# Kernel optimization log

Hardware: AMD Instinct MI355X
Metric: run time of the kernel (lower is better)

Reference implementation:

```python
import jax, jax.numpy as jnp
from jax import lax
import numpy as np

VOCAB, IN_DIM, MEM_DIM, SEQ = 100000, 256, 512, 2048
PAD = 0


def setup_inputs() -> dict:
    key = jax.random.key(0)
    k = jax.random.split(key, 7)
    emb = jax.random.normal(k[0], (VOCAB, IN_DIM), dtype=jnp.float32)
    emb = emb.at[PAD].set(0.0)  # padding_idx row is zero
    s_ih = 1.0 / np.sqrt(IN_DIM)
    s_hh = 1.0 / np.sqrt(MEM_DIM)
    return {
        "linputs": jax.random.randint(k[1], (SEQ,), 0, VOCAB, dtype=jnp.int64),
        "rinputs": jax.random.randint(k[2], (SEQ,), 0, VOCAB, dtype=jnp.int64),
        "emb": emb,
        "W_ih": jax.random.normal(k[3], (4 * MEM_DIM, IN_DIM), dtype=jnp.float32) * s_ih,
        "W_hh": jax.random.normal(k[4], (4 * MEM_DIM, MEM_DIM), dtype=jnp.float32) * s_hh,
        "b_ih": jax.random.normal(k[5], (4 * MEM_DIM,), dtype=jnp.float32) * s_hh,
        "b_hh": jax.random.normal(k[6], (4 * MEM_DIM,), dtype=jnp.float32) * s_hh,
    }


def _lstm_last_h(x_seq, W_ih, W_hh, b):
    # x_seq: [S, in_dim]. Returns h_T [mem_dim]. PyTorch gate order: i, f, g, o.
    H = W_hh.shape[1]
    # precompute input projections for all timesteps (one big GEMM)
    xp = x_seq @ W_ih.T + b  # [S, 4H]
    def step(carry, xg):
        h, c = carry
        gates = xg + h @ W_hh.T  # [4H]
        i = jax.nn.sigmoid(gates[:H])
        f = jax.nn.sigmoid(gates[H:2 * H])
        g = jnp.tanh(gates[2 * H:3 * H])
        o = jax.nn.sigmoid(gates[3 * H:])
        c = f * c + i * g
        h = o * jnp.tanh(c)
        return (h, c), None
    init = (jnp.zeros((H,), x_seq.dtype), jnp.zeros((H,), x_seq.dtype))
    (h, _), _ = lax.scan(step, init, xp)
    return h


def reference(linputs, rinputs, emb, W_ih, W_hh, b_ih, b_hh):
    b = b_ih + b_hh
    lx = emb[linputs]  # [S, in_dim]
    rx = emb[rinputs]
    lh = _lstm_last_h(lx, W_ih, W_hh, b)
    rh = _lstm_last_h(rx, W_ih, W_hh, b)
    return jnp.exp(-jnp.sum(jnp.abs(lh - rh)))
```

## Files before the change

kernel.cpp:

```cpp
#include <hip/hip_runtime.h>
#include <hip/hip_bf16.h>

#define SEQL  2048
#define IND   256
#define MEMD  512
#define G4    2048
#define NWG   16
#define VOCABN 100000

typedef __attribute__((ext_vector_type(4))) unsigned uintx4;
typedef __attribute__((ext_vector_type(2))) _Float16 half2v;

__device__ __forceinline__ unsigned short f2h_bits(float f) {
  _Float16 h = (_Float16)f;
  return __builtin_bit_cast(unsigned short, h);
}
__device__ __forceinline__ float h2f(unsigned bits) {
  return (float)__builtin_bit_cast(_Float16, (unsigned short)(bits & 0xffffu));
}

template <int CTRL>
__device__ __forceinline__ float dpp_fold_add(float v) {
  int x = __builtin_amdgcn_update_dpp(0, __float_as_int(v), CTRL, 0xf, 0xf, true);
  return v + __int_as_float(x);
}

__global__ void init_k(unsigned* __restrict__ hbuf) {
  int i = blockIdx.x * blockDim.x + threadIdx.x;
  if (i < 2 * 2 * MEMD) hbuf[i] = 0u;
}

__global__ __launch_bounds__(256) void xp_gemm(
    const int* __restrict__ lin, const int* __restrict__ rin,
    const float* __restrict__ emb, const float* __restrict__ W_ih,
    const float* __restrict__ b_ih, const float* __restrict__ b_hh,
    unsigned short* __restrict__ xp) {
  __shared__ float As[64][68];
  __shared__ float Bs[64][68];
  const int s = blockIdx.z;
  const int* ids = (s == 0) ? lin : rin;
  const int t0 = blockIdx.x * 64;
  const int n0 = blockIdx.y * 64;
  const int tid = threadIdx.x;
  const int tx = tid & 15, ty = tid >> 4;

  float acc[4][4];
#pragma unroll
  for (int i = 0; i < 4; ++i)
#pragma unroll
    for (int j = 0; j < 4; ++j) acc[i][j] = 0.f;

  for (int kc = 0; kc < IND; kc += 64) {
#pragma unroll
    for (int j = 0; j < 4; ++j) {
      int fi  = tid + 256 * j;
      int row = fi >> 4;
      int c4  = fi & 15;
      int id  = ids[t0 + row];
      id = max(0, min(id, VOCABN - 1));
      const float4 va = *(const float4*)(emb + (size_t)id * IND + kc + c4 * 4);
      As[c4 * 4 + 0][row] = va.x; As[c4 * 4 + 1][row] = va.y;
      As[c4 * 4 + 2][row] = va.z; As[c4 * 4 + 3][row] = va.w;
      const float4 vb = *(const float4*)(W_ih + (size_t)(n0 + row) * IND + kc + c4 * 4);
      Bs[c4 * 4 + 0][row] = vb.x; Bs[c4 * 4 + 1][row] = vb.y;
      Bs[c4 * 4 + 2][row] = vb.z; Bs[c4 * 4 + 3][row] = vb.w;
    }
    __syncthreads();
#pragma unroll 8
    for (int k = 0; k < 64; ++k) {
      const float4 a = *(const float4*)&As[k][tx * 4];
      const float4 b = *(const float4*)&Bs[k][ty * 4];
      acc[0][0] = fmaf(a.x, b.x, acc[0][0]); acc[0][1] = fmaf(a.x, b.y, acc[0][1]);
      acc[0][2] = fmaf(a.x, b.z, acc[0][2]); acc[0][3] = fmaf(a.x, b.w, acc[0][3]);
      acc[1][0] = fmaf(a.y, b.x, acc[1][0]); acc[1][1] = fmaf(a.y, b.y, acc[1][1]);
      acc[1][2] = fmaf(a.y, b.z, acc[1][2]); acc[1][3] = fmaf(a.y, b.w, acc[1][3]);
      acc[2][0] = fmaf(a.z, b.x, acc[2][0]); acc[2][1] = fmaf(a.z, b.y, acc[2][1]);
      acc[2][2] = fmaf(a.z, b.z, acc[2][2]); acc[2][3] = fmaf(a.z, b.w, acc[2][3]);
      acc[3][0] = fmaf(a.w, b.x, acc[3][0]); acc[3][1] = fmaf(a.w, b.y, acc[3][1]);
      acc[3][2] = fmaf(a.w, b.z, acc[3][2]); acc[3][3] = fmaf(a.w, b.w, acc[3][3]);
    }
    __syncthreads();
  }
#pragma unroll
  for (int ri = 0; ri < 4; ++ri) {
#pragma unroll
    for (int bj = 0; bj < 4; ++bj) {
      int t = t0 + tx * 4 + ri;
      int n = n0 + ty * 4 + bj;
      float v = acc[ri][bj] + b_ih[n] + b_hh[n];
      int w = (n & 511) >> 5;
      int gate = n >> 9;
      int hd = n & 31;
      int pos = w * 128 + hd * 4 + gate;
      xp[((size_t)s * SEQL + t) * G4 + pos] = f2h_bits(v);
    }
  }
}

__global__ __launch_bounds__(512, 2) void lstm_rec(
    const float* __restrict__ W_hh,
    const unsigned short* __restrict__ xp,
    unsigned* __restrict__ hbuf) {
  __shared__ unsigned hlds[16 * 20];
  const int blk = blockIdx.x;
  const int s = blk & 1;
  const int w = blk >> 1;
  const int tid = threadIdx.x;
  const int lane = tid & 63;
  const int wv = tid >> 6;
  const int cg = tid & 15;
  const int rg = tid >> 4;

  half2v wreg[4][16];
#pragma unroll
  for (int g = 0; g < 4; ++g) {
    const float* src = W_hh + ((size_t)g * MEMD + w * 32 + rg) * MEMD + cg * 32;
#pragma unroll
    for (int q = 0; q < 8; ++q) {
      const float4 v = *(const float4*)(src + q * 4);
      half2v p0; p0.x = (_Float16)v.x; p0.y = (_Float16)v.y;
      half2v p1; p1.x = (_Float16)v.z; p1.y = (_Float16)v.w;
      wreg[g][q * 2 + 0] = p0;
      wreg[g][q * 2 + 1] = p1;
    }
  }

  unsigned* hbase = hbuf + s * (2 * MEMD);
  const unsigned short* xq0 = xp + (size_t)s * SEQL * G4 + w * 128 + rg * 4;
  float cst = 0.f;

  ushort4 xg_cur = *(const ushort4*)xq0;

  for (int t = 0; t < SEQL; ++t) {
    ushort4 xg_next;
    {
      int tn = (t + 1 < SEQL) ? t + 1 : t;
      xg_next = *(const ushort4*)(xq0 + (size_t)tn * G4);
    }

    if (wv == 0) {
      const unsigned* hr = hbase + (t & 1) * MEMD + 8 * lane;
      unsigned long long a0 = (unsigned long long)hr;
      unsigned long long a1 = (unsigned long long)(hr + 4);
      uintx4 va, vb;
      const unsigned want = (unsigned)t;
      int guard = 0;
      for (;;) {
        asm volatile(
            "global_load_dwordx4 %0, %2, off sc0 sc1\n\t"
            "global_load_dwordx4 %1, %3, off sc0 sc1\n\t"
            "s_waitcnt vmcnt(0)"
            : "=&v"(va), "=&v"(vb)
            : "v"(a0), "v"(a1)
            : "memory");
        bool good = (va.x >> 16) == want && (va.y >> 16) == want &&
                    (va.z >> 16) == want && (va.w >> 16) == want &&
                    (vb.x >> 16) == want && (vb.y >> 16) == want &&
                    (vb.z >> 16) == want && (vb.w >> 16) == want;
        if (__all(good)) break;
        if (++guard > (1 << 16)) break;
      }
      uintx4 pk;
      pk.x = (va.x & 0xffffu) | (va.y << 16);
      pk.y = (va.z & 0xffffu) | (va.w << 16);
      pk.z = (vb.x & 0xffffu) | (vb.y << 16);
      pk.w = (vb.z & 0xffffu) | (vb.w << 16);
      *(uintx4*)&hlds[(lane >> 2) * 20 + (lane & 3) * 4] = pk;
    }
    __syncthreads();

    half2v hp[16];
    {
      const uintx4* hq = (const uintx4*)&hlds[cg * 20];
#pragma unroll
      for (int q = 0; q < 4; ++q) {
        uintx4 u = hq[q];
        hp[q * 4 + 0] = __builtin_bit_cast(half2v, u.x);
        hp[q * 4 + 1] = __builtin_bit_cast(half2v, u.y);
        hp[q * 4 + 2] = __builtin_bit_cast(half2v, u.z);
        hp[q * 4 + 3] = __builtin_bit_cast(half2v, u.w);
      }
    }
    float part[4] = {0.f, 0.f, 0.f, 0.f};
#pragma unroll
    for (int p = 0; p < 16; ++p) {
#pragma unroll
      for (int g = 0; g < 4; ++g)
        part[g] = __builtin_amdgcn_fdot2(wreg[g][p], hp[p], part[g], false);
    }
#pragma unroll
    for (int g = 0; g < 4; ++g) {
      part[g] = dpp_fold_add<0xB1>(part[g]);
      part[g] = dpp_fold_add<0x4E>(part[g]);
      part[g] = dpp_fold_add<0x141>(part[g]);
      part[g] = dpp_fold_add<0x140>(part[g]);
    }

    float gi = part[0] + h2f(xg_cur.x);
    float gf = part[1] + h2f(xg_cur.y);
    float gg = part[2] + h2f(xg_cur.z);
    float go = part[3] + h2f(xg_cur.w);
    float i_ = 1.f / (1.f + __expf(-gi));
    float f_ = 1.f / (1.f + __expf(-gf));
    float ggc = fminf(fmaxf(gg, -15.f), 15.f);
    float e2 = __expf(-2.f * ggc);
    float g_ = (1.f - e2) / (1.f + e2);
    float o_ = 1.f / (1.f + __expf(-go));
    cst = f_ * cst + i_ * g_;
    float cc = fminf(fmaxf(cst, -15.f), 15.f);
    float e2c = __expf(-2.f * cc);
    float th = (1.f - e2c) / (1.f + e2c);
    float h_ = o_ * th;

    unsigned pw = (((unsigned)(t + 1)) << 16) | (unsigned)f2h_bits(h_);
    unsigned q1 = __shfl(pw, 16, 64);
    unsigned q2 = __shfl(pw, 32, 64);
    unsigned q3 = __shfl(pw, 48, 64);
    if (lane == 0) {
      uintx4 val;
      val.x = pw; val.y = q1; val.z = q2; val.w = q3;
      unsigned long long addr =
          (unsigned long long)(hbase + ((t + 1) & 1) * MEMD + w * 32 + wv * 4);
      asm volatile("global_store_dwordx4 %0, %1, off sc0 sc1"
                   :: "v"(addr), "v"(val) : "memory");
    }
    xg_cur = xg_next;
  }
}

__global__ __launch_bounds__(512) void finish_k(const unsigned* __restrict__ hbuf,
                                                float* __restrict__ out) {
  const int tid = threadIdx.x;
  float l = h2f(hbuf[tid]);
  float r = h2f(hbuf[2 * MEMD + tid]);
  float d = fabsf(l - r);
#pragma unroll
  for (int m = 32; m >= 1; m >>= 1) d += __shfl_xor(d, m, 64);
  __shared__ float wsum[8];
  if ((tid & 63) == 0) wsum[tid >> 6] = d;
  __syncthreads();
  if (tid == 0) {
    float sum = 0.f;
#pragma unroll
    for (int i = 0; i < 8; ++i) sum += wsum[i];
    out[0] = expf(-sum);
  }
}

extern "C" void kernel_launch(void* const* d_in, const int* in_sizes, int n_in,
                              void* d_out, int out_size, void* d_ws, size_t ws_size,
                              hipStream_t stream) {
  const int*   lin  = (const int*)d_in[0];
  const int*   rin  = (const int*)d_in[1];
  const float* emb  = (const float*)d_in[2];
  const float* W_ih = (const float*)d_in[3];
  const float* W_hh = (const float*)d_in[4];
  const float* b_ih = (const float*)d_in[5];
  const float* b_hh = (const float*)d_in[6];
  float* out = (float*)d_out;

  unsigned char* ws = (unsigned char*)d_ws;
  unsigned short* xp = (unsigned short*)ws;
  unsigned* hbuf = (unsigned*)(ws + (size_t)2 * SEQL * G4 * sizeof(unsigned short));

  hipLaunchKernelGGL(init_k, dim3(2), dim3(1024), 0, stream, hbuf);
  hipLaunchKernelGGL(xp_gemm, dim3(SEQL / 64, G4 / 64, 2), dim3(256), 0, stream,
                     lin, rin, emb, W_ih, b_ih, b_hh, xp);
  hipLaunchKernelGGL(lstm_rec, dim3(2 * NWG), dim3(512), 0, stream, W_hh, xp, hbuf);
  hipLaunchKernelGGL(finish_k, dim3(1), dim3(512), 0, stream, hbuf, out);
}
```

Measured before the change: 3.661 ms.

## Use 8 workgroups of 1024 threads per sequence for the LSTM recurrence

Each sequence's recurrence now runs on 8 workgroups of 1024 threads instead of 16 of 512. Each workgroup owns 64 hidden units, and the xp gate layout is permuted to match. Halving the number of cooperating workgroups reduces the cross-workgroup polling and synchronisation traffic at every timestep. The hidden-state gather is split across two waves. The cost is larger per-workgroup __syncthreads barriers and higher register pressure at 1024 threads per block.

```diff
diff --git a/kernel.cpp b/kernel.cpp
--- a/kernel.cpp
+++ b/kernel.cpp
@@ -5,7 +5,7 @@
 #define IND   256
 #define MEMD  512
 #define G4    2048
-#define NWG   16
+#define NWGS  8
 #define VOCABN 100000
 
 typedef __attribute__((ext_vector_type(4))) unsigned uintx4;
@@ -88,16 +88,16 @@
       int t = t0 + tx * 4 + ri;
       int n = n0 + ty * 4 + bj;
       float v = acc[ri][bj] + b_ih[n] + b_hh[n];
-      int w = (n & 511) >> 5;
+      int w = (n & 511) >> 6;
       int gate = n >> 9;
-      int hd = n & 31;
-      int pos = w * 128 + hd * 4 + gate;
+      int hd = n & 63;
+      int pos = w * 256 + hd * 4 + gate;
       xp[((size_t)s * SEQL + t) * G4 + pos] = f2h_bits(v);
     }
   }
 }
 
-__global__ __launch_bounds__(512, 2) void lstm_rec(
+__global__ __launch_bounds__(1024, 1) void lstm_rec(
     const float* __restrict__ W_hh,
     const unsigned short* __restrict__ xp,
     unsigned* __restrict__ hbuf) {
@@ -114,7 +114,7 @@
   half2v wreg[4][16];
 #pragma unroll
   for (int g = 0; g < 4; ++g) {
-    const float* src = W_hh + ((size_t)g * MEMD + w * 32 + rg) * MEMD + cg * 32;
+    const float* src = W_hh + ((size_t)g * MEMD + w * 64 + rg) * MEMD + cg * 32;
 #pragma unroll
     for (int q = 0; q < 8; ++q) {
       const float4 v = *(const float4*)(src + q * 4);
@@ -126,10 +126,12 @@
   }
 
   unsigned* hbase = hbuf + s * (2 * MEMD);
-  const unsigned short* xq0 = xp + (size_t)s * SEQL * G4 + w * 128 + rg * 4;
+  const unsigned short* xq0 = xp + (size_t)s * SEQL * G4 + w * 256 + rg * 4;
   float cst = 0.f;
 
   ushort4 xg_cur = *(const ushort4*)xq0;
+
+  const int pidx = wv * 64 + lane;
 
   for (int t = 0; t < SEQL; ++t) {
     ushort4 xg_next;
@@ -138,34 +140,28 @@
       xg_next = *(const ushort4*)(xq0 + (size_t)tn * G4);
     }
 
-    if (wv == 0) {
-      const unsigned* hr = hbase + (t & 1) * MEMD + 8 * lane;
+    if (wv < 2) {
+      const unsigned* hr = hbase + (t & 1) * MEMD + 4 * pidx;
       unsigned long long a0 = (unsigned long long)hr;
-      unsigned long long a1 = (unsigned long long)(hr + 4);
-      uintx4 va, vb;
+      uintx4 va;
       const unsigned want = (unsigned)t;
       int guard = 0;
       for (;;) {
         asm volatile(
-            "global_load_dwordx4 %0, %2, off sc0 sc1\n\t"
-            "global_load_dwordx4 %1, %3, off sc0 sc1\n\t"
+            "global_load_dwordx4 %0, %1, off sc0 sc1\n\t"
             "s_waitcnt vmcnt(0)"
-            : "=&v"(va), "=&v"(vb)
-            : "v"(a0), "v"(a1)
+            : "=&v"(va)
+            : "v"(a0)
             : "memory");
         bool good = (va.x >> 16) == want && (va.y >> 16) == want &&
-                    (va.z >> 16) == want && (va.w >> 16) == want &&
-                    (vb.x >> 16) == want && (vb.y >> 16) == want &&
-                    (vb.z >> 16) == want && (vb.w >> 16) == want;
+                    (va.z >> 16) == want && (va.w >> 16) == want;
         if (__all(good)) break;
         if (++guard > (1 << 16)) break;
       }
-      uintx4 pk;
-      pk.x = (va.x & 0xffffu) | (va.y << 16);
-      pk.y = (va.z & 0xffffu) | (va.w << 16);
-      pk.z = (vb.x & 0xffffu) | (vb.y << 16);
-      pk.w = (vb.z & 0xffffu) | (vb.w << 16);
-      *(uintx4*)&hlds[(lane >> 2) * 20 + (lane & 3) * 4] = pk;
+      unsigned pk0 = (va.x & 0xffffu) | (va.y << 16);
+      unsigned pk1 = (va.z & 0xffffu) | (va.w << 16);
+      unsigned* dst = &hlds[(pidx >> 3) * 20 + (pidx & 7) * 2];
+      dst[0] = pk0; dst[1] = pk1;
     }
     __syncthreads();
 
@@ -220,7 +216,7 @@
       uintx4 val;
       val.x = pw; val.y = q1; val.z = q2; val.w = q3;
       unsigned long long addr =
-          (unsigned long long)(hbase + ((t + 1) & 1) * MEMD + w * 32 + wv * 4);
+          (unsigned long long)(hbase + ((t + 1) & 1) * MEMD + w * 64 + wv * 4);
       asm volatile("global_store_dwordx4 %0, %1, off sc0 sc1"
                    :: "v"(addr), "v"(val) : "memory");
     }
@@ -266,6 +262,6 @@
   hipLaunchKernelGGL(init_k, dim3(2), dim3(1024), 0, stream, hbuf);
   hipLaunchKernelGGL(xp_gemm, dim3(SEQL / 64, G4 / 64, 2), dim3(256), 0, stream,
                      lin, rin, emb, W_ih, b_ih, b_hh, xp);
-  hipLaunchKernelGGL(lstm_rec, dim3(2 * NWG), dim3(512), 0, stream, W_hh, xp, hbuf);
+  hipLaunchKernelGGL(lstm_rec, dim3(2 * NWGS), dim3(1024), 0, stream, W_hh, xp, hbuf);
   hipLaunchKernelGGL(finish_k, dim3(1), dim3(512), 0, stream, hbuf, out);
 }
```

Measured after the change: 5.028 ms. 1.37x slower.

## Give each consumer workgroup a private h mailbox written by all producers

Applied to the files above, without the earlier changes.

Each workgroup now writes its new h slice to 16 separate per-consumer mailboxes instead of one shared buffer. Every consumer then polls only its own private copy. The aim is to cut contention and cache-line sharing when 16 workgroups spin on the same lines each timestep. In exchange, each producer issues 16 times as many system-coherent stores, and the mailbox region is 16 times larger to initialise.

```diff
diff --git a/kernel.cpp b/kernel.cpp
--- a/kernel.cpp
+++ b/kernel.cpp
@@ -8,6 +8,9 @@
 #define NWG   16
 #define VOCABN 100000
 
+#define MB_SEQ   (NWG * 2 * MEMD)
+#define MB_CONS  (2 * MEMD)
+
 typedef __attribute__((ext_vector_type(4))) unsigned uintx4;
 typedef __attribute__((ext_vector_type(2))) _Float16 half2v;
 
@@ -25,9 +28,9 @@
   return v + __int_as_float(x);
 }
 
-__global__ void init_k(unsigned* __restrict__ hbuf) {
+__global__ void init_k(unsigned* __restrict__ mb) {
   int i = blockIdx.x * blockDim.x + threadIdx.x;
-  if (i < 2 * 2 * MEMD) hbuf[i] = 0u;
+  if (i < 2 * MB_SEQ) mb[i] = 0u;
 }
 
 __global__ __launch_bounds__(256) void xp_gemm(
@@ -100,7 +103,7 @@
 __global__ __launch_bounds__(512, 2) void lstm_rec(
     const float* __restrict__ W_hh,
     const unsigned short* __restrict__ xp,
-    unsigned* __restrict__ hbuf) {
+    unsigned* __restrict__ mb) {
   __shared__ unsigned hlds[16 * 20];
   const int blk = blockIdx.x;
   const int s = blk & 1;
@@ -125,7 +128,8 @@
     }
   }
 
-  unsigned* hbase = hbuf + s * (2 * MEMD);
+  unsigned* mbs = mb + s * MB_SEQ;
+  unsigned* mymb = mbs + w * MB_CONS;
   const unsigned short* xq0 = xp + (size_t)s * SEQL * G4 + w * 128 + rg * 4;
   float cst = 0.f;
 
@@ -139,7 +143,7 @@
     }
 
     if (wv == 0) {
-      const unsigned* hr = hbase + (t & 1) * MEMD + 8 * lane;
+      const unsigned* hr = mymb + (t & 1) * MEMD + 8 * lane;
       unsigned long long a0 = (unsigned long long)hr;
       unsigned long long a1 = (unsigned long long)(hr + 4);
       uintx4 va, vb;
@@ -216,11 +220,11 @@
     unsigned q1 = __shfl(pw, 16, 64);
     unsigned q2 = __shfl(pw, 32, 64);
     unsigned q3 = __shfl(pw, 48, 64);
-    if (lane == 0) {
+    if (lane < 16) {
       uintx4 val;
       val.x = pw; val.y = q1; val.z = q2; val.w = q3;
-      unsigned long long addr =
-          (unsigned long long)(hbase + ((t + 1) & 1) * MEMD + w * 32 + wv * 4);
+      unsigned long long addr = (unsigned long long)(
+          mbs + lane * MB_CONS + ((t + 1) & 1) * MEMD + w * 32 + wv * 4);
       asm volatile("global_store_dwordx4 %0, %1, off sc0 sc1"
                    :: "v"(addr), "v"(val) : "memory");
     }
@@ -228,11 +232,11 @@
   }
 }
 
-__global__ __launch_bounds__(512) void finish_k(const unsigned* __restrict__ hbuf,
+__global__ __launch_bounds__(512) void finish_k(const unsigned* __restrict__ mb,
                                                 float* __restrict__ out) {
   const int tid = threadIdx.x;
-  float l = h2f(hbuf[tid]);
-  float r = h2f(hbuf[2 * MEMD + tid]);
+  float l = h2f(mb[tid]);
+  float r = h2f(mb[MB_SEQ + tid]);
   float d = fabsf(l - r);
 #pragma unroll
   for (int m = 32; m >= 1; m >>= 1) d += __shfl_xor(d, m, 64);
@@ -261,11 +265,11 @@
 
   unsigned char* ws = (unsigned char*)d_ws;
   unsigned short* xp = (unsigned short*)ws;
-  unsigned* hbuf = (unsigned*)(ws + (size_t)2 * SEQL * G4 * sizeof(unsigned short));
-
-  hipLaunchKernelGGL(init_k, dim3(2), dim3(1024), 0, stream, hbuf);
+  unsigned* mb = (unsigned*)(ws + (size_t)2 * SEQL * G4 * sizeof(unsigned short));
+
+  hipLaunchKernelGGL(init_k, dim3(2 * MB_SEQ / 1024), dim3(1024), 0, stream, mb);
   hipLaunchKernelGGL(xp_gemm, dim3(SEQL / 64, G4 / 64, 2), dim3(256), 0, stream,
                      lin, rin, emb, W_ih, b_ih, b_hh, xp);
-  hipLaunchKernelGGL(lstm_rec, dim3(2 * NWG), dim3(512), 0, stream, W_hh, xp, hbuf);
-  hipLaunchKernelGGL(finish_k, dim3(1), dim3(512), 0, stream, hbuf, out);
-}
+  hipLaunchKernelGGL(lstm_rec, dim3(2 * NWG), dim3(512), 0, stream, W_hh, xp, mb);
+  hipLaunchKernelGGL(finish_k, dim3(1), dim3(512), 0, stream, mb, out);
+}
```

Result: no change. 3.590 ms (median of 2 runs) (-1.9%).
